# Kernel tuning notes

Hardware: AMD Instinct MI355X
Metric: run time of the kernel (lower is better)

The kernel has to match this reference:

```python
import jax, jax.numpy as jnp
import numpy as np
import math

B, T, C, H, L, V = 16, 512, 1024, 16, 4, 32000
D = C // H


def setup_inputs() -> dict:
    key = jax.random.key(0)
    ks = jax.random.split(key, 10)
    X = jax.random.randint(ks[0], (B, T), 0, V)
    S = jax.random.bernoulli(ks[1], 0.5, (B, T)).astype(jnp.int32)
    # I + S must equal 1 everywhere, else get_attn_mask fully masks a row -> NaN softmax
    I = (1 - S).astype(jnp.float32)
    s = 0.02
    emb_table = jax.random.normal(ks[2], (V + 1, C), jnp.float32) * s
    pos_emb = jax.random.normal(ks[3], (T, C), jnp.float32) * s
    qkv_w = jax.random.normal(ks[4], (L, 3 * C, C), jnp.float32) * s
    out_w = jax.random.normal(ks[5], (L, C, C), jnp.float32) * s
    ffn_w1 = jax.random.normal(ks[6], (L, C, C), jnp.float32) * s
    ffn_b1 = jnp.zeros((L, C), jnp.float32)
    ffn_w2 = jax.random.normal(ks[7], (L, C, C), jnp.float32) * s
    ffn_b2 = jnp.zeros((L, C), jnp.float32)
    return dict(X=X, I=I, S=S, emb_table=emb_table, pos_emb=pos_emb,
                qkv_w=qkv_w, out_w=out_w, ffn_w1=ffn_w1, ffn_b1=ffn_b1,
                ffn_w2=ffn_w2, ffn_b2=ffn_b2)


def _forward(X, I, S, emb_table, pos_emb, qkv_w, out_w, ffn_w1, ffn_b1, ffn_w2, ffn_b2):
    # token_to_embeddings: unobserved (S==0) tokens remapped to sentinel index V
    Xm = X * S + (1 - S) * V                      # [B,T]
    x = emb_table[Xm] + pos_emb[None]             # [B,T,C]
    # additive mask from outer product of validity flags m = I + S
    m = I + S.astype(I.dtype)                     # [B,T]
    prod = m[:, :, None] * m[:, None, :]          # [B,T,T]
    bias = jnp.where(prod == 1.0, 0.0, -jnp.inf)[:, None]  # [B,1,T,T]
    scale = 1.0 / math.sqrt(D)
    for i in range(L):
        wq, wk, wv = qkv_w[i, :C], qkv_w[i, C:2 * C], qkv_w[i, 2 * C:]
        q = (x @ wq.T).reshape(B, T, H, D)
        k = (x @ wk.T).reshape(B, T, H, D)
        v = (x @ wv.T).reshape(B, T, H, D)
        scores = jnp.einsum('bqhd,bkhd->bhqk', q * scale, k) + bias
        attn = jax.nn.softmax(scores, axis=-1)
        o = jnp.einsum('bhqk,bkhd->bqhd', attn, v).reshape(B, T, C)
        x = o @ out_w[i].T + x                    # out projection + residual
        h = jax.nn.relu(x @ ffn_w1[i].T + ffn_b1[i])
        x = x + (h @ ffn_w2[i].T + ffn_b2[i])
    # readout: bmm(x^T, I) -> [B,C]
    return jnp.einsum('btc,bt->bc', x, I)


def reference(X, I, S, emb_table, pos_emb, qkv_w, out_w, ffn_w1, ffn_b1, ffn_w2, ffn_b2):
    return _forward(X, I, S, emb_table, pos_emb, qkv_w, out_w,
                    ffn_w1, ffn_b1, ffn_w2, ffn_b2)
```

## Files before the change

kernel.cpp:

```cpp
#include <hip/hip_runtime.h>
#include <stdint.h>

#define LAYERS 4
#define BB 16
#define TT 512
#define CC 1024
#define HH 16
#define DD 64
#define VV 32000
#define MM (BB*TT)

typedef __attribute__((ext_vector_type(8))) short bf16x8;
typedef __attribute__((ext_vector_type(4))) float f32x4;
typedef __attribute__((ext_vector_type(16))) float f32x16;

__device__ __forceinline__ unsigned short f2b(float f) {
  union { float f; unsigned int u; } v; v.f = f;
  unsigned int r = v.u + 0x7FFFu + ((v.u >> 16) & 1u);
  return (unsigned short)(r >> 16);
}
__device__ __forceinline__ float blo(unsigned int u) {
  union { unsigned int x; float f; } v; v.x = u << 16; return v.f;
}
__device__ __forceinline__ float bhi(unsigned int u) {
  union { unsigned int x; float f; } v; v.x = u & 0xFFFF0000u; return v.f;
}
__device__ __forceinline__ uint32_t pkbf(float lo, float hi) {
  uint32_t d; asm("v_cvt_pk_bf16_f32 %0, %1, %2" : "=v"(d) : "v"(lo), "v"(hi)); return d;
}
__device__ __forceinline__ float ex2(float x) {
  float r; asm("v_exp_f32 %0, %1" : "=v"(r) : "v"(x)); return r;
}
__device__ __forceinline__ void gload16(const unsigned short* g, const unsigned short* lds) {
  __builtin_amdgcn_global_load_lds((const __attribute__((address_space(1))) void*)g,
                                   (__attribute__((address_space(3))) void*)lds, 16, 0, 0);
}

__global__ __launch_bounds__(256) void cvt_kernel(const float* __restrict__ src,
                                                  unsigned short* __restrict__ dst, int n4) {
  int i = blockIdx.x * 256 + threadIdx.x;
  if (i >= n4) return;
  float4 v = ((const float4*)src)[i];
  ushort4 o; o.x = f2b(v.x); o.y = f2b(v.y); o.z = f2b(v.z); o.w = f2b(v.w);
  ((ushort4*)dst)[i] = o;
}

__global__ __launch_bounds__(256) void embed_kernel(const int* __restrict__ X, const int* __restrict__ S,
    const float* __restrict__ emb, const float* __restrict__ pos,
    float* __restrict__ x, unsigned short* __restrict__ xb) {
  int bt = blockIdx.x; int tid = threadIdx.x;
  int t = bt & (TT - 1);
  int tok = S[bt] ? X[bt] : VV;
  float4 e = ((const float4*)(emb + (size_t)tok * CC))[tid];
  float4 p = ((const float4*)(pos + (size_t)t * CC))[tid];
  float4 r; r.x = e.x + p.x; r.y = e.y + p.y; r.z = e.z + p.z; r.w = e.w + p.w;
  ((float4*)(x + (size_t)bt * CC))[tid] = r;
  ushort4 ub; ub.x = f2b(r.x); ub.y = f2b(r.y); ub.z = f2b(r.z); ub.w = f2b(r.w);
  ((ushort4*)(xb + (size_t)bt * CC))[tid] = ub;
}

template<int EPI>
__global__ __launch_bounds__(256, 2) void gemm6_kernel(
    const unsigned short* __restrict__ A,
    const unsigned short* __restrict__ W,
    float* __restrict__ xres,
    unsigned short* __restrict__ outb,
    const float* __restrict__ bias,
    int N, int nbx) {
  extern __shared__ unsigned short lds[];
  const int K = 1024;
  const int tid = threadIdx.x;
  const int wv = tid >> 6, ln = tid & 63;
  const int g = ln >> 4, rr = ln & 15;
  const int wm = wv >> 1, wn = wv & 1;

  const int nwg = gridDim.x;
  const int bid = blockIdx.x;
  const int swz = (bid & 7) * (nwg >> 3) + (bid >> 3);
  const int by = swz / nbx, bx = swz - by * nbx;
  const int brow = by * 256, bcol = bx * 128;

  const unsigned short* asrc[4];
  const unsigned short* bsrc[2];
  #pragma unroll
  for (int rd = 0; rd < 4; ++rd)
    asrc[rd] = A + (size_t)(brow + rd * 64 + (tid >> 2)) * K + (tid & 3) * 8;
  #pragma unroll
  for (int rd = 0; rd < 2; ++rd)
    bsrc[rd] = W + (size_t)(bcol + rd * 64 + (tid >> 2)) * K + (tid & 3) * 8;

  auto stage = [&](int tile, int buf) {
    unsigned short* Ad = lds + buf * 12288 + wv * 512;
    unsigned short* Bd = lds + buf * 12288 + 8192 + wv * 512;
    int ko = tile * 32;
    #pragma unroll
    for (int rd = 0; rd < 4; ++rd) gload16(asrc[rd] + ko, Ad + rd * 2048);
    #pragma unroll
    for (int rd = 0; rd < 2; ++rd) gload16(bsrc[rd] + ko, Bd + rd * 2048);
  };

  f32x4 acc[8][4];
  #pragma unroll
  for (int i = 0; i < 8; ++i)
    #pragma unroll
    for (int j = 0; j < 4; ++j)
      acc[i][j] = (f32x4){0.f, 0.f, 0.f, 0.f};

  stage(0, 0);
  stage(1, 1);
  asm volatile("s_waitcnt vmcnt(6)" ::: "memory");
  __builtin_amdgcn_s_barrier();

  int bufc = 0;
  for (int t = 0; t < 32; ++t) {
    int bufn = bufc + 2; if (bufn >= 3) bufn -= 3;
    if (t < 30) {
      stage(t + 2, bufn);
      asm volatile("s_waitcnt vmcnt(12)" ::: "memory");
    } else if (t == 30) {
      asm volatile("s_waitcnt vmcnt(6)" ::: "memory");
    } else {
      asm volatile("s_waitcnt vmcnt(0)" ::: "memory");
    }
    __builtin_amdgcn_s_barrier();
    __builtin_amdgcn_sched_barrier(0);

    const unsigned short* Ab = lds + bufc * 12288;
    const unsigned short* Bb = Ab + 8192;
    bf16x8 av[8], bv[4];
    #pragma unroll
    for (int i = 0; i < 8; ++i)
      av[i] = *(const bf16x8*)(Ab + (wm * 128 + i * 16 + rr) * 32 + g * 8);
    #pragma unroll
    for (int j = 0; j < 4; ++j)
      bv[j] = *(const bf16x8*)(Bb + (wn * 64 + j * 16 + rr) * 32 + g * 8);

    __builtin_amdgcn_s_setprio(1);
    #pragma unroll
    for (int i = 0; i < 8; ++i)
      #pragma unroll
      for (int j = 0; j < 4; ++j)
        acc[i][j] = __builtin_amdgcn_mfma_f32_16x16x32_bf16(av[i], bv[j], acc[i][j], 0, 0, 0);
    __builtin_amdgcn_s_setprio(0);
    __builtin_amdgcn_sched_barrier(0);
    __builtin_amdgcn_s_barrier();
    bufc += 1; if (bufc == 3) bufc = 0;
  }

  #pragma unroll
  for (int i = 0; i < 8; ++i) {
    #pragma unroll
    for (int j = 0; j < 4; ++j) {
      #pragma unroll
      for (int q = 0; q < 4; ++q) {
        int rowg = brow + wm * 128 + i * 16 + g * 4 + q;
        int colg = bcol + wn * 64 + j * 16 + rr;
        size_t off = (size_t)rowg * N + colg;
        float vacc = acc[i][j][q];
        if (EPI == 0) {
          outb[off] = f2b(vacc);
        } else if (EPI == 1) {
          float nx = xres[off] + vacc;
          xres[off] = nx; outb[off] = f2b(nx);
        } else if (EPI == 2) {
          float hv = vacc + bias[colg];
          hv = hv > 0.f ? hv : 0.f;
          outb[off] = f2b(hv);
        } else {
          float nx = xres[off] + vacc + bias[colg];
          xres[off] = nx; outb[off] = f2b(nx);
        }
      }
    }
  }
}

template<int E>
__device__ __forceinline__ bf16x8 buildP(const f32x16& p) {
  uint32_t a = pkbf(p[E + 0], p[E + 1]);
  uint32_t b = pkbf(p[E + 4], p[E + 5]);
  uint32_t c = pkbf(p[E + 2], p[E + 3]);
  uint32_t d = pkbf(p[E + 6], p[E + 7]);
  asm("v_permlane32_swap_b32 %0, %1" : "+v"(a), "+v"(b));
  asm("v_permlane32_swap_b32 %0, %1" : "+v"(c), "+v"(d));
  union { uint32_t u[4]; bf16x8 v; } r;
  r.u[0] = a; r.u[1] = c; r.u[2] = b; r.u[3] = d;
  return r.v;
}

__global__ __launch_bounds__(256) void attn_kernel(const unsigned short* __restrict__ qkv,
                                                   unsigned short* __restrict__ ob) {
  __shared__ unsigned short Kl[64 * 64];
  __shared__ unsigned short Vt[64 * 64];
  const int tid = threadIdx.x;
  const int wv = tid >> 6, ln = tid & 63;
  const int lq = ln & 31, hi = ln >> 5;
  const int qt = blockIdx.x >> 8, bh = blockIdx.x & 255;
  const int b = bh >> 4, h = bh & 15;
  const int qrow = qt * 128 + wv * 32 + lq;
  const size_t rowQ = (size_t)(b * TT + qrow) * 3072 + h * 64;

  const float cs = 0.125f * 1.44269504f;
  bf16x8 qf[4];
  #pragma unroll
  for (int t = 0; t < 4; ++t) {
    uint4 u = *(const uint4*)(qkv + rowQ + t * 16 + hi * 8);
    uint32_t w[4] = {u.x, u.y, u.z, u.w};
    union { uint32_t u4[4]; bf16x8 v; } cv;
    #pragma unroll
    for (int j = 0; j < 4; ++j) cv.u4[j] = pkbf(blo(w[j]) * cs, bhi(w[j]) * cs);
    qf[t] = cv.v;
  }

  f32x16 o0 = {}, o1 = {};
  float mrun = -3.0e38f, lsum = 0.f;

  for (int kv0 = 0; kv0 < TT; kv0 += 64) {
    if (kv0) __syncthreads();
    #pragma unroll
    for (int r = 0; r < 2; ++r) {
      int ch = r * 256 + tid;
      int k = ch >> 3, cc = ch & 7;
      int sg = (k & 7) ^ (k >> 3);
      const unsigned short* gs = qkv + (size_t)(b * TT + kv0 + k) * 3072 + 1024 + h * 64 + ((cc ^ sg) << 3);
      gload16(gs, Kl + (size_t)(r * 256 + wv * 64) * 8);
    }
    {
      int cc = tid & 7, kp = tid >> 3;
      int k = kp * 2;
      const unsigned short* gv = qkv + (size_t)(b * TT + kv0 + k) * 3072 + 2048 + h * 64 + cc * 8;
      uint4 g1 = *(const uint4*)gv;
      uint4 g2 = *(const uint4*)(gv + 3072);
      uint32_t w1[4] = {g1.x, g1.y, g1.z, g1.w}, w2[4] = {g2.x, g2.y, g2.z, g2.w};
      #pragma unroll
      for (int j = 0; j < 8; ++j) {
        int d = cc * 8 + j;
        uint32_t dw = (j & 1) ? ((w1[j >> 1] >> 16) | (w2[j >> 1] & 0xFFFF0000u))
                              : ((w1[j >> 1] & 0xFFFFu) | (w2[j >> 1] << 16));
        int sg = (d & 7) ^ (d >> 3);
        *(uint32_t*)(Vt + d * 64 + (k ^ (sg << 3))) = dw;
      }
    }
    __syncthreads();

    f32x16 s0 = {}, s1 = {};
    #pragma unroll
    for (int t = 0; t < 4; ++t) {
      int r0 = lq, r1 = 32 + lq;
      bf16x8 a0 = *(const bf16x8*)(Kl + r0 * 64 + ((((t << 1) | hi) ^ ((r0 & 7) ^ (r0 >> 3))) << 3));
      bf16x8 a1 = *(const bf16x8*)(Kl + r1 * 64 + ((((t << 1) | hi) ^ ((r1 & 7) ^ (r1 >> 3))) << 3));
      s0 = __builtin_amdgcn_mfma_f32_32x32x16_bf16(a0, qf[t], s0, 0, 0, 0);
      s1 = __builtin_amdgcn_mfma_f32_32x32x16_bf16(a1, qf[t], s1, 0, 0, 0);
    }

    float mx = s0[0];
    #pragma unroll
    for (int r = 1; r < 16; ++r) mx = fmaxf(mx, s0[r]);
    #pragma unroll
    for (int r = 0; r < 16; ++r) mx = fmaxf(mx, s1[r]);
    mx = fmaxf(mx, __shfl_xor(mx, 32));
    float mnew = fmaxf(mrun, mx);
    float cf = ex2(mrun - mnew);
    mrun = mnew;
    lsum *= cf;
    #pragma unroll
    for (int r = 0; r < 16; ++r) { o0[r] *= cf; o1[r] *= cf; }
    #pragma unroll
    for (int r = 0; r < 16; ++r) {
      s0[r] = ex2(s0[r] - mnew);
      s1[r] = ex2(s1[r] - mnew);
      lsum += s0[r] + s1[r];
    }

    bf16x8 pf0 = buildP<0>(s0);
    bf16x8 pf1 = buildP<8>(s0);
    bf16x8 pf2 = buildP<0>(s1);
    bf16x8 pf3 = buildP<8>(s1);

    #pragma unroll
    for (int t = 0; t < 4; ++t) {
      bf16x8 pf = (t == 0) ? pf0 : (t == 1) ? pf1 : (t == 2) ? pf2 : pf3;
      int d0 = lq, d1 = 32 + lq;
      bf16x8 v0 = *(const bf16x8*)(Vt + d0 * 64 + ((((t << 1) | hi) ^ ((d0 & 7) ^ (d0 >> 3))) << 3));
      bf16x8 v1 = *(const bf16x8*)(Vt + d1 * 64 + ((((t << 1) | hi) ^ ((d1 & 7) ^ (d1 >> 3))) << 3));
      o0 = __builtin_amdgcn_mfma_f32_32x32x16_bf16(v0, pf, o0, 0, 0, 0);
      o1 = __builtin_amdgcn_mfma_f32_32x32x16_bf16(v1, pf, o1, 0, 0, 0);
    }
  }

  lsum += __shfl_xor(lsum, 32);
  float inv = 1.f / lsum;
  size_t orow = (size_t)(b * TT + qrow) * CC + h * 64;
  #pragma unroll
  for (int md = 0; md < 2; ++md) {
    #pragma unroll
    for (int rq = 0; rq < 4; ++rq) {
      int d0 = md * 32 + rq * 8 + hi * 4;
      float e0 = (md ? o1[rq * 4 + 0] : o0[rq * 4 + 0]) * inv;
      float e1 = (md ? o1[rq * 4 + 1] : o0[rq * 4 + 1]) * inv;
      float e2 = (md ? o1[rq * 4 + 2] : o0[rq * 4 + 2]) * inv;
      float e3 = (md ? o1[rq * 4 + 3] : o0[rq * 4 + 3]) * inv;
      uint2 st; st.x = pkbf(e0, e1); st.y = pkbf(e2, e3);
      *(uint2*)(ob + orow + d0) = st;
    }
  }
}

__global__ __launch_bounds__(256) void final_kernel(const float* __restrict__ x,
                                                    const float* __restrict__ I,
                                                    float* __restrict__ out) {
  int b = blockIdx.x >> 2;
  int c = ((blockIdx.x & 3) << 8) + threadIdx.x;
  float acc = 0.f;
  const float* xp = x + (size_t)b * TT * CC + c;
  const float* Ip = I + (size_t)b * TT;
  for (int t = 0; t < TT; ++t) acc = fmaf(xp[(size_t)t * CC], Ip[t], acc);
  out[b * CC + c] = acc;
}

extern "C" void kernel_launch(void* const* d_in, const int* in_sizes, int n_in,
                              void* d_out, int out_size, void* d_ws, size_t ws_size,
                              hipStream_t stream) {
  const int*   X      = (const int*)d_in[0];
  const float* I      = (const float*)d_in[1];
  const int*   S      = (const int*)d_in[2];
  const float* emb    = (const float*)d_in[3];
  const float* pos    = (const float*)d_in[4];
  const float* qkv_w  = (const float*)d_in[5];
  const float* out_w  = (const float*)d_in[6];
  const float* ffn_w1 = (const float*)d_in[7];
  const float* ffn_b1 = (const float*)d_in[8];
  const float* ffn_w2 = (const float*)d_in[9];
  const float* ffn_b2 = (const float*)d_in[10];
  float* out = (float*)d_out;

  char* ws = (char*)d_ws;
  size_t off = 0;
  auto walloc = [&](size_t bytes) { char* p = ws + off; off += (bytes + 255) & ~(size_t)255; return p; };
  unsigned short* wqkv = (unsigned short*)walloc((size_t)LAYERS * 3 * CC * CC * 2);
  unsigned short* wo   = (unsigned short*)walloc((size_t)LAYERS * CC * CC * 2);
  unsigned short* w1   = (unsigned short*)walloc((size_t)LAYERS * CC * CC * 2);
  unsigned short* w2   = (unsigned short*)walloc((size_t)LAYERS * CC * CC * 2);
  float*          x    = (float*)walloc((size_t)MM * CC * 4);
  unsigned short* xb   = (unsigned short*)walloc((size_t)MM * CC * 2);
  unsigned short* qkvb = (unsigned short*)walloc((size_t)MM * 3 * CC * 2);
  unsigned short* obuf = (unsigned short*)walloc((size_t)MM * CC * 2);
  unsigned short* hbuf = (unsigned short*)walloc((size_t)MM * CC * 2);
  if (off > ws_size) return;

  int n4;
  n4 = LAYERS * 3 * CC * CC / 4; cvt_kernel<<<(n4 + 255) / 256, 256, 0, stream>>>(qkv_w, wqkv, n4);
  n4 = LAYERS * CC * CC / 4;     cvt_kernel<<<(n4 + 255) / 256, 256, 0, stream>>>(out_w, wo, n4);
  n4 = LAYERS * CC * CC / 4;     cvt_kernel<<<(n4 + 255) / 256, 256, 0, stream>>>(ffn_w1, w1, n4);
  n4 = LAYERS * CC * CC / 4;     cvt_kernel<<<(n4 + 255) / 256, 256, 0, stream>>>(ffn_w2, w2, n4);

  embed_kernel<<<MM, 256, 0, stream>>>(X, S, emb, pos, x, xb);

  const size_t ldsB = 72 * 1024;
  for (int l = 0; l < LAYERS; ++l) {
    gemm6_kernel<0><<<(MM / 256) * (3 * CC / 128), 256, ldsB, stream>>>(
        xb, wqkv + (size_t)l * 3 * CC * CC, nullptr, qkvb, nullptr, 3 * CC, 3 * CC / 128);
    attn_kernel<<<4 * 256, 256, 0, stream>>>(qkvb, obuf);
    gemm6_kernel<1><<<(MM / 256) * (CC / 128), 256, ldsB, stream>>>(
        obuf, wo + (size_t)l * CC * CC, x, xb, nullptr, CC, CC / 128);
    gemm6_kernel<2><<<(MM / 256) * (CC / 128), 256, ldsB, stream>>>(
        xb, w1 + (size_t)l * CC * CC, nullptr, hbuf, ffn_b1 + l * CC, CC, CC / 128);
    gemm6_kernel<3><<<(MM / 256) * (CC / 128), 256, ldsB, stream>>>(
        hbuf, w2 + (size_t)l * CC * CC, x, xb, ffn_b2 + l * CC, CC, CC / 128);
  }

  final_kernel<<<BB * 4, 256, 0, stream>>>(x, I, out);
}
```

Measured before the change: 926.4 us.

## Restructure GEMM to 512-thread blocks with swizzled LDS and smaller tiles

```diff
diff --git a/kernel.cpp b/kernel.cpp
--- a/kernel.cpp
+++ b/kernel.cpp
@@ -59,14 +59,17 @@
   ((ushort4*)(xb + (size_t)bt * CC))[tid] = ub;
 }
 
-template<int EPI>
-__global__ __launch_bounds__(256, 2) void gemm6_kernel(
+template<int EPI, int BM>
+__global__ __launch_bounds__(512, 4) void gemm8_kernel(
     const unsigned short* __restrict__ A,
     const unsigned short* __restrict__ W,
     float* __restrict__ xres,
     unsigned short* __restrict__ outb,
     const float* __restrict__ bias,
     int N, int nbx) {
+  constexpr int NA = BM / 128;
+  constexpr int MI = BM / 64;
+  constexpr int BUFS = (BM + 128) * 32;
   extern __shared__ unsigned short lds[];
   const int K = 1024;
   const int tid = threadIdx.x;
@@ -78,82 +81,79 @@
   const int bid = blockIdx.x;
   const int swz = (bid & 7) * (nwg >> 3) + (bid >> 3);
   const int by = swz / nbx, bx = swz - by * nbx;
-  const int brow = by * 256, bcol = bx * 128;
-
-  const unsigned short* asrc[4];
-  const unsigned short* bsrc[2];
-  #pragma unroll
-  for (int rd = 0; rd < 4; ++rd)
-    asrc[rd] = A + (size_t)(brow + rd * 64 + (tid >> 2)) * K + (tid & 3) * 8;
-  #pragma unroll
-  for (int rd = 0; rd < 2; ++rd)
-    bsrc[rd] = W + (size_t)(bcol + rd * 64 + (tid >> 2)) * K + (tid & 3) * 8;
+  const int brow = by * BM, bcol = bx * 128;
+
+  const unsigned short* asrc[NA];
+  #pragma unroll
+  for (int rd = 0; rd < NA; ++rd) {
+    int p = rd * 512 + tid;
+    int row = p >> 2, gg = p & 3;
+    asrc[rd] = A + (size_t)(brow + row) * K + (gg ^ ((row >> 1) & 3)) * 8;
+  }
+  const unsigned short* bsrc;
+  {
+    int row = tid >> 2, gg = tid & 3;
+    bsrc = W + (size_t)(bcol + row) * K + (gg ^ ((row >> 1) & 3)) * 8;
+  }
 
   auto stage = [&](int tile, int buf) {
-    unsigned short* Ad = lds + buf * 12288 + wv * 512;
-    unsigned short* Bd = lds + buf * 12288 + 8192 + wv * 512;
+    unsigned short* Aba = lds + buf * BUFS;
+    unsigned short* Bba = Aba + BM * 32;
     int ko = tile * 32;
     #pragma unroll
-    for (int rd = 0; rd < 4; ++rd) gload16(asrc[rd] + ko, Ad + rd * 2048);
-    #pragma unroll
-    for (int rd = 0; rd < 2; ++rd) gload16(bsrc[rd] + ko, Bd + rd * 2048);
+    for (int rd = 0; rd < NA; ++rd)
+      gload16(asrc[rd] + ko, Aba + (rd * 512 + wv * 64) * 8);
+    gload16(bsrc + ko, Bba + (wv * 64) * 8);
   };
 
-  f32x4 acc[8][4];
-  #pragma unroll
-  for (int i = 0; i < 8; ++i)
+  f32x4 acc[MI][4];
+  #pragma unroll
+  for (int i = 0; i < MI; ++i)
     #pragma unroll
     for (int j = 0; j < 4; ++j)
       acc[i][j] = (f32x4){0.f, 0.f, 0.f, 0.f};
 
   stage(0, 0);
-  stage(1, 1);
-  asm volatile("s_waitcnt vmcnt(6)" ::: "memory");
-  __builtin_amdgcn_s_barrier();
-
-  int bufc = 0;
+
+  const int chx = (g ^ ((rr >> 1) & 3)) * 8;
   for (int t = 0; t < 32; ++t) {
-    int bufn = bufc + 2; if (bufn >= 3) bufn -= 3;
-    if (t < 30) {
-      stage(t + 2, bufn);
-      asm volatile("s_waitcnt vmcnt(12)" ::: "memory");
-    } else if (t == 30) {
-      asm volatile("s_waitcnt vmcnt(6)" ::: "memory");
+    if (t < 31) {
+      stage(t + 1, (t + 1) & 1);
+      asm volatile("s_waitcnt vmcnt(%0)" :: "i"(NA + 1) : "memory");
     } else {
       asm volatile("s_waitcnt vmcnt(0)" ::: "memory");
     }
     __builtin_amdgcn_s_barrier();
     __builtin_amdgcn_sched_barrier(0);
 
-    const unsigned short* Ab = lds + bufc * 12288;
-    const unsigned short* Bb = Ab + 8192;
-    bf16x8 av[8], bv[4];
-    #pragma unroll
-    for (int i = 0; i < 8; ++i)
-      av[i] = *(const bf16x8*)(Ab + (wm * 128 + i * 16 + rr) * 32 + g * 8);
+    const unsigned short* Aba = lds + (t & 1) * BUFS;
+    const unsigned short* Bba = Aba + BM * 32;
+    bf16x8 av[MI], bv[4];
+    #pragma unroll
+    for (int i = 0; i < MI; ++i)
+      av[i] = *(const bf16x8*)(Aba + (wm * (BM / 4) + i * 16 + rr) * 32 + chx);
     #pragma unroll
     for (int j = 0; j < 4; ++j)
-      bv[j] = *(const bf16x8*)(Bb + (wn * 64 + j * 16 + rr) * 32 + g * 8);
+      bv[j] = *(const bf16x8*)(Bba + (wn * 64 + j * 16 + rr) * 32 + chx);
 
     __builtin_amdgcn_s_setprio(1);
     #pragma unroll
-    for (int i = 0; i < 8; ++i)
+    for (int i = 0; i < MI; ++i)
       #pragma unroll
       for (int j = 0; j < 4; ++j)
         acc[i][j] = __builtin_amdgcn_mfma_f32_16x16x32_bf16(av[i], bv[j], acc[i][j], 0, 0, 0);
     __builtin_amdgcn_s_setprio(0);
     __builtin_amdgcn_sched_barrier(0);
     __builtin_amdgcn_s_barrier();
-    bufc += 1; if (bufc == 3) bufc = 0;
-  }
-
-  #pragma unroll
-  for (int i = 0; i < 8; ++i) {
+  }
+
+  #pragma unroll
+  for (int i = 0; i < MI; ++i) {
     #pragma unroll
     for (int j = 0; j < 4; ++j) {
       #pragma unroll
       for (int q = 0; q < 4; ++q) {
-        int rowg = brow + wm * 128 + i * 16 + g * 4 + q;
+        int rowg = brow + wm * (BM / 4) + i * 16 + g * 4 + q;
         int colg = bcol + wn * 64 + j * 16 + rr;
         size_t off = (size_t)rowg * N + colg;
         float vacc = acc[i][j][q];
@@ -356,16 +356,17 @@
 
   embed_kernel<<<MM, 256, 0, stream>>>(X, S, emb, pos, x, xb);
 
-  const size_t ldsB = 72 * 1024;
+  const size_t lds256 = 2 * (256 + 128) * 32 * 2;
+  const size_t lds128 = 2 * (128 + 128) * 32 * 2;
   for (int l = 0; l < LAYERS; ++l) {
-    gemm6_kernel<0><<<(MM / 256) * (3 * CC / 128), 256, ldsB, stream>>>(
+    gemm8_kernel<0, 256><<<(MM / 256) * (3 * CC / 128), 512, lds256, stream>>>(
         xb, wqkv + (size_t)l * 3 * CC * CC, nullptr, qkvb, nullptr, 3 * CC, 3 * CC / 128);
     attn_kernel<<<4 * 256, 256, 0, stream>>>(qkvb, obuf);
-    gemm6_kernel<1><<<(MM / 256) * (CC / 128), 256, ldsB, stream>>>(
+    gemm8_kernel<1, 128><<<(MM / 128) * (CC / 128), 512, lds128, stream>>>(
         obuf, wo + (size_t)l * CC * CC, x, xb, nullptr, CC, CC / 128);
-    gemm6_kernel<2><<<(MM / 256) * (CC / 128), 256, ldsB, stream>>>(
+    gemm8_kernel<2, 128><<<(MM / 128) * (CC / 128), 512, lds128, stream>>>(
         xb, w1 + (size_t)l * CC * CC, nullptr, hbuf, ffn_b1 + l * CC, CC, CC / 128);
-    gemm6_kernel<3><<<(MM / 256) * (CC / 128), 256, ldsB, stream>>>(
+    gemm8_kernel<3, 128><<<(MM / 128) * (CC / 128), 512, lds128, stream>>>(
         hbuf, w2 + (size_t)l * CC * CC, x, xb, ffn_b2 + l * CC, CC, CC / 128);
   }
 
```

Result: faster. 779.9 us (-15.8%).
